# Kernel tuning notes

Hardware: AMD Instinct MI355X
Metric: run time of the kernel (lower is better)

## Reference

```python
import jax, jax.numpy as jnp
import numpy as np

B, N, D = 8, 2048, 256
K = 8
NP = 1024  # num_pooled = ceil(N * 0.5)
EPS = 1e-8
TEMP = 1.0


def setup_inputs() -> dict:
    key = jax.random.key(0)
    k1, k2, k3, k4 = jax.random.split(key, 4)
    tokens = jax.random.normal(k1, (B, N, D), dtype=jnp.float32)
    timestamps = jax.random.uniform(k2, (B, N), dtype=jnp.float32)
    W1 = jax.random.normal(k3, (2 * D, 128), dtype=jnp.float32) * 0.02
    b1 = jnp.zeros((128,), dtype=jnp.float32)
    W2 = jax.random.normal(k4, (128, NP), dtype=jnp.float32) * 0.02
    b2 = jnp.zeros((NP,), dtype=jnp.float32)
    return {"tokens": tokens, "timestamps": timestamps, "W1": W1, "b1": b1, "W2": W2, "b2": b2}


def _build_adjacency(tokens):
    # mutual-kNN graph on cosine similarity -> [B, N, N] float 0/1
    tn = tokens / (jnp.linalg.norm(tokens, axis=-1, keepdims=True) + EPS)
    sim = jnp.einsum("bnd,bmd->bnm", tn, tn)
    sim = jnp.where(jnp.eye(N, dtype=bool)[None], -jnp.inf, sim)  # no self (add_self=False)
    _, idx = jax.lax.top_k(sim, K)  # [B, N, K]
    bi = jnp.arange(B)[:, None, None]
    ri = jnp.arange(N)[None, :, None]
    adj = jnp.zeros((B, N, N), dtype=bool).at[bi, ri, idx].set(True)
    adj = adj & jnp.swapaxes(adj, 1, 2)  # mutual
    return adj.astype(jnp.float32)


def reference(tokens, timestamps, W1, b1, W2, b2):
    adjacency = _build_adjacency(tokens)

    # degree-normalized aggregation (use_gnn=True)
    degree = jnp.clip(adjacency.sum(axis=-1, keepdims=True), 1.0, None)
    agg = jnp.matmul(adjacency / degree, tokens)  # [B, N, D]
    features = jnp.concatenate([tokens, agg], axis=-1)  # [B, N, 2D]

    # assignment MLP (Linear -> exact GELU -> Linear), softmax over clusters
    h = jax.nn.gelu(features @ W1 + b1, approximate=False)
    logits = h @ W2 + b2  # [B, N, NP]
    assign = jax.nn.softmax(logits / TEMP, axis=-1)

    # soft-assignment pooling
    pooled_tokens = jnp.einsum("bnp,bnd->bpd", assign, tokens)  # [B, NP, D]
    pooled_t = jnp.einsum("bnp,bn->bp", assign, timestamps)  # [B, NP]

    # reorder pooled tokens by pooled timestamp
    sort_idx = jnp.argsort(pooled_t, axis=-1)
    pooled_tokens = jnp.take_along_axis(pooled_tokens, sort_idx[..., None], axis=1)
    pooled_t = jnp.take_along_axis(pooled_t, sort_idx, axis=1)

    # auxiliary losses
    assign_st = jnp.einsum("bnp,bmp->bnm", assign, assign)
    link_loss = jnp.mean((assign_st - adjacency) ** 2)
    entropy = jnp.mean(-jnp.sum(assign * jnp.log(assign + EPS), axis=-1))

    return pooled_tokens, pooled_t, link_loss, entropy
```

## Files before the change

### kernel.cpp

```cpp
#include <hip/hip_runtime.h>
#include <math.h>

#define B_ 8
#define N_ 2048
#define D_ 256
#define K_ 8
#define NP_ 1024
#define H_ 128
#define EPS_ 1e-8f
#define NEG_INF_ (-1e30f)

typedef unsigned int uint;
typedef unsigned short ushort;
typedef __attribute__((ext_vector_type(4))) float f32x4;
typedef __attribute__((ext_vector_type(8))) short short8;

__device__ __forceinline__ float gelu_exact(float x) {
    return 0.5f * x * (1.0f + erff(x * 0.70710678118654752440f));
}

__device__ __forceinline__ float dot4(float4 a, float4 b) {
    return a.x * b.x + a.y * b.y + a.z * b.z + a.w * b.w;
}

__device__ __forceinline__ ushort f2bf(float f) {
    uint u = __float_as_uint(f);
    u = (u + 0x7FFFu + ((u >> 16) & 1u)) >> 16;
    return (ushort)u;
}

__device__ __forceinline__ void gll16(const void* g, void* l) {
    __builtin_amdgcn_global_load_lds(
        (const __attribute__((address_space(1))) unsigned int*)g,
        (__attribute__((address_space(3))) unsigned int*)l, 16, 0, 0);
}

__device__ __forceinline__ float bsum256(float* red, int t, float v) {
    red[t] = v;
    __syncthreads();
#pragma unroll
    for (int s = 128; s > 0; s >>= 1) {
        if (t < s) red[t] += red[t + s];
        __syncthreads();
    }
    float r = red[0];
    __syncthreads();
    return r;
}

__device__ __forceinline__ float bmax256(float* red, int t, float v) {
    red[t] = v;
    __syncthreads();
#pragma unroll
    for (int s = 128; s > 0; s >>= 1) {
        if (t < s) red[t] = fmaxf(red[t], red[t + s]);
        __syncthreads();
    }
    float r = red[0];
    __syncthreads();
    return r;
}

__device__ __forceinline__ uint mono16(uint v) {
    return (v & 0x8000u) ? ((~v) & 0xFFFFu) : (v | 0x8000u);
}

__global__ __launch_bounds__(256) void k_norm(const float* __restrict__ tokens,
                                              float* __restrict__ tn,
                                              ushort* __restrict__ tnbf) {
    int row = blockIdx.x;
    int t = threadIdx.x;
    __shared__ float red[256];
    float x = tokens[(size_t)row * D_ + t];
    float ss = bsum256(red, t, x * x);
    float nrm = sqrtf(ss) + EPS_;
    float y = x / nrm;
    tn[(size_t)row * D_ + t] = y;
    tnbf[(size_t)row * D_ + t] = f2bf(y);
}

#define SCW_ 72
#define INSK_(L) { bool in_ = key > L; uint tm_ = L; L = in_ ? key : L; key = in_ ? tm_ : key; }
#define INS16_ INSK_(l0) INSK_(l1) INSK_(l2) INSK_(l3) INSK_(l4) INSK_(l5) INSK_(l6) INSK_(l7) \
               INSK_(l8) INSK_(l9) INSK_(l10) INSK_(l11) INSK_(l12) INSK_(l13) INSK_(l14) INSK_(l15)
#define INSM_ INSK_(m0) INSK_(m1) INSK_(m2) INSK_(m3) INSK_(m4) INSK_(m5) INSK_(m6) INSK_(m7) \
              INSK_(m8) INSK_(m9) INSK_(m10) INSK_(m11) INSK_(m12) INSK_(m13) INSK_(m14) INSK_(m15)

__global__ __launch_bounds__(256) void k_simtop(const ushort* __restrict__ tnbf,
                                                int* __restrict__ cands) {
    __shared__ __align__(16) char lds[43264];
    char* Bs = lds + 8192;
    ushort* sc = (ushort*)(lds + 40960);
    uint* mg = (uint*)(lds + 8192);

    int bid = blockIdx.x;
    int b = bid & 7;
    int panel = bid >> 3;
    int i0 = panel * 16;
    int t = threadIdx.x;
    int lane = t & 63;
    int wv = t >> 6;
    const char* tbb = (const char*)(tnbf + (size_t)b * N_ * D_);

#pragma unroll
    for (int c = 0; c < 2; ++c) {
        int e = (wv * 2 + c) * 64 + lane;
        int row = e >> 5, g = e & 31;
        gll16(tbb + (size_t)(i0 + row) * 512 + ((g ^ (row & 15)) << 4),
              lds + (wv * 2 + c) * 1024);
    }
#pragma unroll
    for (int c = 0; c < 8; ++c) {
        int e = (wv * 8 + c) * 64 + lane;
        int row = e >> 5, g = e & 31;
        gll16(tbb + (size_t)row * 512 + ((g ^ (row & 15)) << 4),
              Bs + (wv * 8 + c) * 1024);
    }
    asm volatile("s_waitcnt vmcnt(0)" ::: "memory");
    __syncthreads();

    int selrow = t >> 4;
    int selcs = t & 15;
    int gi = i0 + selrow;
    uint l0=0,l1=0,l2=0,l3=0,l4=0,l5=0,l6=0,l7=0,l8=0,l9=0,l10=0,l11=0,l12=0,l13=0,l14=0,l15=0;

    int arow = lane & 15;
    int brow = wv * 16 + (lane & 15);
    int scw = ((lane >> 4) * 4) * SCW_ + wv * 16 + (lane & 15);

    for (int jt = 0; jt < 32; ++jt) {
        f32x4 acc = (f32x4){0.f, 0.f, 0.f, 0.f};
#pragma unroll
        for (int ks = 0; ks < 8; ++ks) {
            int u = ks * 4 + (lane >> 4);
            short8 af = *(const short8*)(lds + arow * 512 + ((u ^ arow) << 4));
            short8 bf = *(const short8*)(Bs + brow * 512 + ((u ^ (lane & 15)) << 4));
            acc = __builtin_amdgcn_mfma_f32_16x16x32_bf16(af, bf, acc, 0, 0, 0);
        }
#pragma unroll
        for (int v = 0; v < 4; ++v) sc[scw + v * SCW_] = f2bf(acc[v]);
        __syncthreads();

        if (jt < 31) {
#pragma unroll
            for (int c = 0; c < 8; ++c) {
                int e = (wv * 8 + c) * 64 + lane;
                int row = e >> 5, g = e & 31;
                gll16(tbb + (size_t)((jt + 1) * 64 + row) * 512 + ((g ^ (row & 15)) << 4),
                      Bs + (wv * 8 + c) * 1024);
            }
        }
        int j0 = jt * 64;
        int sbase = selrow * SCW_;
#pragma unroll
        for (int jj = 0; jj < 4; ++jj) {
            int col = selcs + jj * 16;
            int j = j0 + col;
            uint sv = sc[sbase + col];
            if (j != gi) {
                uint key = (mono16(sv) << 16) | (65535u - (uint)j);
                if (key > l15) { INS16_ }
            }
        }
        asm volatile("s_waitcnt vmcnt(0)" ::: "memory");
        __syncthreads();
    }

    uint* ml = mg + (size_t)t * 17;
    ml[0]=l0; ml[1]=l1; ml[2]=l2; ml[3]=l3; ml[4]=l4; ml[5]=l5; ml[6]=l6; ml[7]=l7;
    ml[8]=l8; ml[9]=l9; ml[10]=l10; ml[11]=l11; ml[12]=l12; ml[13]=l13; ml[14]=l14; ml[15]=l15;
    __syncthreads();
    if (selcs == 0) {
        uint m0=0,m1=0,m2=0,m3=0,m4=0,m5=0,m6=0,m7=0,m8=0,m9=0,m10=0,m11=0,m12=0,m13=0,m14=0,m15=0;
        const uint* base = mg + (size_t)(selrow * 16) * 17;
#pragma unroll
        for (int s2 = 0; s2 < 16; ++s2) {
            const uint* lp = base + s2 * 17;
            for (int q = 0; q < 16; ++q) {
                uint key = lp[q];
                if (key <= m15) break;
                INSM_
            }
        }
        int* crow = cands + ((size_t)b * N_ + gi) * 16;
        crow[0]=(int)(65535u-(m0&0xFFFFu));   crow[1]=(int)(65535u-(m1&0xFFFFu));
        crow[2]=(int)(65535u-(m2&0xFFFFu));   crow[3]=(int)(65535u-(m3&0xFFFFu));
        crow[4]=(int)(65535u-(m4&0xFFFFu));   crow[5]=(int)(65535u-(m5&0xFFFFu));
        crow[6]=(int)(65535u-(m6&0xFFFFu));   crow[7]=(int)(65535u-(m7&0xFFFFu));
        crow[8]=(int)(65535u-(m8&0xFFFFu));   crow[9]=(int)(65535u-(m9&0xFFFFu));
        crow[10]=(int)(65535u-(m10&0xFFFFu)); crow[11]=(int)(65535u-(m11&0xFFFFu));
        crow[12]=(int)(65535u-(m12&0xFFFFu)); crow[13]=(int)(65535u-(m13&0xFFFFu));
        crow[14]=(int)(65535u-(m14&0xFFFFu)); crow[15]=(int)(65535u-(m15&0xFFFFu));
    }
}

__global__ __launch_bounds__(64) void k_rescore(const float* __restrict__ tn,
                                                const int* __restrict__ cands,
                                                int* __restrict__ topk) {
    int row = blockIdx.x;
    int b = row >> 11;
    int lane = threadIdx.x;
    int j = cands[(size_t)row * 16 + (lane & 15)];
    float s = 0.f;
    if (lane < 16) {
        const float* ti = tn + (size_t)row * D_;
        const float* tj = tn + ((size_t)(b << 11) + j) * D_;
        for (int d = 0; d < D_; d += 4) {
            float4 u = *(const float4*)(tj + d);
            float4 w = *(const float4*)(ti + d);
            s += dot4(u, w);
        }
    }
    float dv[16];
    int jv[16];
#pragma unroll
    for (int c = 0; c < 16; ++c) {
        dv[c] = __shfl(s, c);
        jv[c] = __shfl(j, c);
    }
    uint used = 0;
    for (int r = 0; r < 8; ++r) {
        float bv = -1e38f;
        int bj = 1 << 30, bc = -1;
#pragma unroll
        for (int c = 0; c < 16; ++c) {
            bool av = !(used & (1u << c));
            bool better = av && (dv[c] > bv || (dv[c] == bv && jv[c] < bj));
            bv = better ? dv[c] : bv;
            bj = better ? jv[c] : bj;
            bc = better ? c : bc;
        }
        used |= 1u << bc;
        if (lane == 0) topk[(size_t)row * K_ + r] = bj;
    }
}

__global__ __launch_bounds__(64) void k_adj_agg(const float* __restrict__ tokens,
                                                const int* __restrict__ topk,
                                                int* __restrict__ nbr,
                                                int* __restrict__ deg,
                                                float* __restrict__ agg) {
    int row = blockIdx.x;
    int b = row >> 11;
    int i = row & (N_ - 1);
    int t = threadIdx.x;
    __shared__ int s_cand[K_];
    __shared__ int s_nbr[K_];
    __shared__ int s_deg;
    if (t < K_) {
        int j = topk[(size_t)row * K_ + t];
        const int* tj = topk + ((size_t)(b * N_ + j)) * K_;
        bool mut = false;
#pragma unroll
        for (int k = 0; k < K_; ++k) mut = mut || (tj[k] == i);
        s_cand[t] = mut ? j : -1;
    }
    __syncthreads();
    if (t == 0) {
        int d = 0;
#pragma unroll
        for (int k = 0; k < K_; ++k)
            if (s_cand[k] >= 0) s_nbr[d++] = s_cand[k];
        s_deg = d;
    }
    __syncthreads();
    int dgi = s_deg;
    const float* tb = tokens + (size_t)b * N_ * D_;
    float a0 = 0, a1 = 0, a2 = 0, a3 = 0;
    for (int k = 0; k < dgi; ++k) {
        float4 v = *(const float4*)(tb + (size_t)s_nbr[k] * D_ + t * 4);
        a0 += v.x; a1 += v.y; a2 += v.z; a3 += v.w;
    }
    float inv = 1.0f / (float)(dgi > 0 ? dgi : 1);
    *(float4*)(agg + (size_t)row * D_ + t * 4) = make_float4(a0 * inv, a1 * inv, a2 * inv, a3 * inv);
    if (t < K_) nbr[(size_t)row * K_ + t] = (t < dgi) ? s_nbr[t] : -1;
    if (t == 0) deg[row] = dgi;
}

__global__ __launch_bounds__(256) void k_tokT(const float* __restrict__ tokens,
                                              ushort* __restrict__ tokT) {
    int b = blockIdx.z;
    int n0 = blockIdx.x * 32, d0 = blockIdx.y * 32;
    __shared__ float tile[32][33];
    int t = threadIdx.x;
#pragma unroll
    for (int q = 0; q < 4; ++q) {
        int e = q * 256 + t;
        int r = e >> 5, c = e & 31;
        tile[r][c] = tokens[((size_t)b * N_ + n0 + r) * D_ + d0 + c];
    }
    __syncthreads();
#pragma unroll
    for (int q = 0; q < 4; ++q) {
        int e = q * 256 + t;
        int r = e >> 5, c = e & 31;
        tokT[((size_t)b * D_ + d0 + r) * N_ + n0 + c] = f2bf(tile[c][r]);
    }
}

__global__ __launch_bounds__(256) void k_asT(const float* __restrict__ assign,
                                             ushort* __restrict__ assignT) {
    int b = blockIdx.z;
    int n0 = blockIdx.x * 32, p0 = blockIdx.y * 32;
    __shared__ float tile[32][33];
    int t = threadIdx.x;
#pragma unroll
    for (int q = 0; q < 4; ++q) {
        int e = q * 256 + t;
        int r = e >> 5, c = e & 31;
        tile[r][c] = assign[((size_t)b * N_ + n0 + r) * NP_ + p0 + c];
    }
    __syncthreads();
#pragma unroll
    for (int q = 0; q < 4; ++q) {
        int e = q * 256 + t;
        int r = e >> 5, c = e & 31;
        assignT[((size_t)b * NP_ + p0 + r) * N_ + n0 + c] = f2bf(tile[c][r]);
    }
}

__global__ __launch_bounds__(256) void k_mlp1(const float* __restrict__ tokens,
                                              const float* __restrict__ agg,
                                              const float* __restrict__ W1,
                                              const float* __restrict__ b1,
                                              float* __restrict__ h) {
    int row0 = blockIdx.x * 16;
    int t = threadIdx.x;
    int col = t & 127;
    int half = t >> 7;
    __shared__ float feat[16][2 * D_];
    for (int e = t; e < 16 * 2 * D_; e += 256) {
        int r = e >> 9, c = e & 511;
        feat[r][c] = (c < D_) ? tokens[(size_t)(row0 + r) * D_ + c]
                              : agg[(size_t)(row0 + r) * D_ + (c - D_)];
    }
    __syncthreads();
    const float* fr = &feat[half * 8][0];
    float bias = b1[col];
    float a0 = bias, a1 = bias, a2 = bias, a3 = bias, a4 = bias, a5 = bias, a6 = bias, a7 = bias;
    for (int i = 0; i < 2 * D_; i += 4) {
        float w0 = W1[(size_t)(i + 0) * H_ + col];
        float w1 = W1[(size_t)(i + 1) * H_ + col];
        float w2 = W1[(size_t)(i + 2) * H_ + col];
        float w3 = W1[(size_t)(i + 3) * H_ + col];
        float4 f0 = *(const float4*)(fr + 0 * 512 + i);
        float4 f1 = *(const float4*)(fr + 1 * 512 + i);
        float4 f2 = *(const float4*)(fr + 2 * 512 + i);
        float4 f3 = *(const float4*)(fr + 3 * 512 + i);
        float4 f4 = *(const float4*)(fr + 4 * 512 + i);
        float4 f5 = *(const float4*)(fr + 5 * 512 + i);
        float4 f6 = *(const float4*)(fr + 6 * 512 + i);
        float4 f7 = *(const float4*)(fr + 7 * 512 + i);
        a0 += f0.x * w0; a0 += f0.y * w1; a0 += f0.z * w2; a0 += f0.w * w3;
        a1 += f1.x * w0; a1 += f1.y * w1; a1 += f1.z * w2; a1 += f1.w * w3;
        a2 += f2.x * w0; a2 += f2.y * w1; a2 += f2.z * w2; a2 += f2.w * w3;
        a3 += f3.x * w0; a3 += f3.y * w1; a3 += f3.z * w2; a3 += f3.w * w3;
        a4 += f4.x * w0; a4 += f4.y * w1; a4 += f4.z * w2; a4 += f4.w * w3;
        a5 += f5.x * w0; a5 += f5.y * w1; a5 += f5.z * w2; a5 += f5.w * w3;
        a6 += f6.x * w0; a6 += f6.y * w1; a6 += f6.z * w2; a6 += f6.w * w3;
        a7 += f7.x * w0; a7 += f7.y * w1; a7 += f7.z * w2; a7 += f7.w * w3;
    }
    int rb = row0 + half * 8;
    h[(size_t)(rb + 0) * H_ + col] = gelu_exact(a0);
    h[(size_t)(rb + 1) * H_ + col] = gelu_exact(a1);
    h[(size_t)(rb + 2) * H_ + col] = gelu_exact(a2);
    h[(size_t)(rb + 3) * H_ + col] = gelu_exact(a3);
    h[(size_t)(rb + 4) * H_ + col] = gelu_exact(a4);
    h[(size_t)(rb + 5) * H_ + col] = gelu_exact(a5);
    h[(size_t)(rb + 6) * H_ + col] = gelu_exact(a6);
    h[(size_t)(rb + 7) * H_ + col] = gelu_exact(a7);
}

__global__ __launch_bounds__(256) void k_mlp2f(const float* __restrict__ hmat,
                                               const float* __restrict__ W2,
                                               const float* __restrict__ b2,
                                               float* __restrict__ assign,
                                               float* __restrict__ ent_partial) {
    int row0 = blockIdx.x * 16;
    int t = threadIdx.x;
    __shared__ float hsT[128 * 17];
    __shared__ float red2[16][256];
    __shared__ float red[256];
    for (int e = t; e < 16 * H_; e += 256) {
        int r = e >> 7, i = e & 127;
        hsT[i * 17 + r] = hmat[(size_t)row0 * H_ + e];
    }
    __syncthreads();
    float acc[16][4];
#pragma unroll
    for (int s = 0; s < 4; ++s) {
        float bb = b2[s * 256 + t];
#pragma unroll
        for (int r = 0; r < 16; ++r) acc[r][s] = bb;
    }
#pragma unroll 2
    for (int i = 0; i < H_; ++i) {
        float w0 = W2[(size_t)i * NP_ + t];
        float w1 = W2[(size_t)i * NP_ + 256 + t];
        float w2 = W2[(size_t)i * NP_ + 512 + t];
        float w3 = W2[(size_t)i * NP_ + 768 + t];
        float hv[16];
        *(float4*)&hv[0] = *(const float4*)&hsT[i * 17 + 0];
        *(float4*)&hv[4] = *(const float4*)&hsT[i * 17 + 4];
        *(float4*)&hv[8] = *(const float4*)&hsT[i * 17 + 8];
        *(float4*)&hv[12] = *(const float4*)&hsT[i * 17 + 12];
#pragma unroll
        for (int r = 0; r < 16; ++r) {
            acc[r][0] += hv[r] * w0; acc[r][1] += hv[r] * w1;
            acc[r][2] += hv[r] * w2; acc[r][3] += hv[r] * w3;
        }
    }
#pragma unroll
    for (int r = 0; r < 16; ++r)
        red2[r][t] = fmaxf(fmaxf(acc[r][0], acc[r][1]), fmaxf(acc[r][2], acc[r][3]));
    __syncthreads();
#pragma unroll
    for (int s = 128; s > 0; s >>= 1) {
        if (t < s) {
#pragma unroll
            for (int r = 0; r < 16; ++r) red2[r][t] = fmaxf(red2[r][t], red2[r][t + s]);
        }
        __syncthreads();
    }
#pragma unroll
    for (int r = 0; r < 16; ++r) {
        float m = red2[r][0];
        acc[r][0] -= m; acc[r][1] -= m; acc[r][2] -= m; acc[r][3] -= m;
    }
    __syncthreads();
#pragma unroll
    for (int r = 0; r < 16; ++r)
        red2[r][t] = expf(acc[r][0]) + expf(acc[r][1]) + expf(acc[r][2]) + expf(acc[r][3]);
    __syncthreads();
#pragma unroll
    for (int s = 128; s > 0; s >>= 1) {
        if (t < s) {
#pragma unroll
            for (int r = 0; r < 16; ++r) red2[r][t] += red2[r][t + s];
        }
        __syncthreads();
    }
    float entv = 0.f;
#pragma unroll
    for (int r = 0; r < 16; ++r) {
        float tot = red2[r][0];
        float inv = 1.0f / tot;
        float p0 = expf(acc[r][0]) * inv, p1 = expf(acc[r][1]) * inv;
        float p2 = expf(acc[r][2]) * inv, p3 = expf(acc[r][3]) * inv;
        float* arow = assign + (size_t)(row0 + r) * NP_;
        arow[t] = p0; arow[256 + t] = p1; arow[512 + t] = p2; arow[768 + t] = p3;
        entv -= p0 * logf(p0 + EPS_) + p1 * logf(p1 + EPS_) + p2 * logf(p2 + EPS_) + p3 * logf(p3 + EPS_);
    }
    float bs = bsum256(red, t, entv);
    if (t == 0) ent_partial[blockIdx.x] = bs;
}

__device__ __forceinline__ void stage8k(const ushort* __restrict__ A,
                                        const ushort* __restrict__ B,
                                        int kb, char* lA, char* lB, int wv, int lane) {
#pragma unroll
    for (int c = 0; c < 2; ++c) {
        int e = (wv * 2 + c) * 64 + lane;
        int row = e >> 3, g = e & 7;
        size_t go = (size_t)row * N_ + kb + ((g ^ (row & 7)) << 3);
        gll16(A + go, lA + (wv * 2 + c) * 1024);
        gll16(B + go, lB + (wv * 2 + c) * 1024);
    }
}

__device__ __forceinline__ void gemm64g(const ushort* __restrict__ A,
                                        const ushort* __restrict__ B,
                                        f32x4 acc[2][2], char* lds) {
    int t = threadIdx.x;
    int lane = t & 63;
    int wv = t >> 6;
    int wm = wv >> 1, wn = wv & 1;
    stage8k(A, B, 0, lds, lds + 8192, wv, lane);
    for (int kb = 0; kb < N_; kb += 64) {
        int cur = (kb >> 6) & 1;
        char* lA = lds + cur * 16384;
        char* lB = lA + 8192;
        asm volatile("s_waitcnt vmcnt(0)" ::: "memory");
        __syncthreads();
        if (kb + 64 < N_) {
            char* nA = lds + (cur ^ 1) * 16384;
            stage8k(A, B, kb + 64, nA, nA + 8192, wv, lane);
        }
#pragma unroll
        for (int ks = 0; ks < 2; ++ks) {
            short8 afr[2], bfr[2];
#pragma unroll
            for (int f = 0; f < 2; ++f) {
                int rowA = wm * 32 + f * 16 + (lane & 15);
                int u = ks * 4 + (lane >> 4);
                afr[f] = *(const short8*)(lA + rowA * 128 + ((u ^ (rowA & 7)) << 4));
                int rowB = wn * 32 + f * 16 + (lane & 15);
                bfr[f] = *(const short8*)(lB + rowB * 128 + ((u ^ (rowB & 7)) << 4));
            }
#pragma unroll
            for (int fm = 0; fm < 2; ++fm)
#pragma unroll
                for (int fn = 0; fn < 2; ++fn)
                    acc[fm][fn] = __builtin_amdgcn_mfma_f32_16x16x32_bf16(
                        afr[fm], bfr[fn], acc[fm][fn], 0, 0, 0);
        }
    }
}

__global__ __launch_bounds__(256) void k_pool64(const ushort* __restrict__ assignT,
                                                const ushort* __restrict__ tokT,
                                                float* __restrict__ pooled) {
    __shared__ __align__(16) char lds[32768];
    int bid = blockIdx.x;
    int b = bid & 7;
    int tile = bid >> 3;
    int p0 = (tile >> 2) * 64, d0 = (tile & 3) * 64;
    const ushort* A = assignT + ((size_t)b * NP_ + p0) * N_;
    const ushort* Bp = tokT + ((size_t)b * D_ + d0) * N_;
    f32x4 acc[2][2];
#pragma unroll
    for (int x = 0; x < 2; ++x)
#pragma unroll
        for (int y = 0; y < 2; ++y) acc[x][y] = (f32x4){0.f, 0.f, 0.f, 0.f};
    gemm64g(A, Bp, acc, lds);
    int lane = threadIdx.x & 63;
    int wid = threadIdx.x >> 6;
    int wm = wid >> 1, wn = wid & 1;
#pragma unroll
    for (int fm = 0; fm < 2; ++fm)
#pragma unroll
        for (int fn = 0; fn < 2; ++fn) {
            int p = p0 + wm * 32 + fm * 16 + (lane >> 4) * 4;
            int d = d0 + wn * 32 + fn * 16 + (lane & 15);
#pragma unroll
            for (int v = 0; v < 4; ++v)
                pooled[((size_t)b * NP_ + p + v) * D_ + d] = acc[fm][fn][v];
        }
}

__global__ __launch_bounds__(256) void k_gram64(const ushort* __restrict__ assignT,
                                                float* __restrict__ gram_partial) {
    __shared__ __align__(16) char lds[32768];
    __shared__ float red[256];
    int bid = blockIdx.x;
    int b = bid & 7;
    int idx = bid >> 3;
    int ti = 0, rem = idx;
    while (rem >= 16 - ti) { rem -= 16 - ti; ++ti; }
    int tj = ti + rem;
    const ushort* A = assignT + ((size_t)b * NP_ + ti * 64) * N_;
    const ushort* Bp = assignT + ((size_t)b * NP_ + tj * 64) * N_;
    f32x4 acc[2][2];
#pragma unroll
    for (int x = 0; x < 2; ++x)
#pragma unroll
        for (int y = 0; y < 2; ++y) acc[x][y] = (f32x4){0.f, 0.f, 0.f, 0.f};
    gemm64g(A, Bp, acc, lds);
    float lsum = 0.f;
#pragma unroll
    for (int x = 0; x < 2; ++x)
#pragma unroll
        for (int y = 0; y < 2; ++y)
#pragma unroll
            for (int v = 0; v < 4; ++v) lsum += acc[x][y][v] * acc[x][y][v];
    float bs = bsum256(red, threadIdx.x, lsum);
    if (threadIdx.x == 0) gram_partial[(size_t)b * 136 + idx] = (ti == tj ? 1.0f : 2.0f) * bs;
}

__global__ __launch_bounds__(256) void k_poolt_part(const float* __restrict__ assign,
                                                    const float* __restrict__ ts,
                                                    float* __restrict__ part) {
    int bid = blockIdx.x;
    int b = bid & 7, ck = bid >> 3;
    int t = threadIdx.x;
    const float* A = assign + ((size_t)b * N_ + (size_t)ck * 64) * NP_;
    const float* T = ts + (size_t)b * N_ + (size_t)ck * 64;
    float4 acc = make_float4(0.f, 0.f, 0.f, 0.f);
    for (int n = 0; n < 64; ++n) {
        float4 v = *(const float4*)(A + (size_t)n * NP_ + t * 4);
        float tv = T[n];
        acc.x += v.x * tv; acc.y += v.y * tv; acc.z += v.z * tv; acc.w += v.w * tv;
    }
    *(float4*)(part + ((size_t)(b * 32 + ck)) * NP_ + t * 4) = acc;
}

__global__ __launch_bounds__(256) void k_poolt_red(const float* __restrict__ part,
                                                   float* __restrict__ pooled_t_u) {
    int b = blockIdx.x;
    int t = threadIdx.x;
    float4 acc = make_float4(0.f, 0.f, 0.f, 0.f);
    for (int ck = 0; ck < 32; ++ck) {
        float4 v = *(const float4*)(part + ((size_t)(b * 32 + ck)) * NP_ + t * 4);
        acc.x += v.x; acc.y += v.y; acc.z += v.z; acc.w += v.w;
    }
    *(float4*)(pooled_t_u + (size_t)b * NP_ + t * 4) = acc;
}

__global__ __launch_bounds__(64) void k_edge(const float* __restrict__ assign,
                                             const int* __restrict__ nbr,
                                             const int* __restrict__ deg,
                                             float* __restrict__ edge_partial) {
    int row = blockIdx.x;
    int t = threadIdx.x;
    int dgi = deg[row];
    int b = row >> 11;
    float acc = 0.f;
    if (dgi > 0) {
        const float* ai = assign + (size_t)row * NP_;
        float areg[16];
#pragma unroll
        for (int q = 0; q < 16; ++q) areg[q] = ai[q * 64 + t];
        for (int k = 0; k < dgi; ++k) {
            int j = nbr[(size_t)row * K_ + k];
            const float* aj = assign + ((size_t)(b * N_ + j)) * NP_;
#pragma unroll
            for (int q = 0; q < 16; ++q) acc += areg[q] * aj[q * 64 + t];
        }
    }
#pragma unroll
    for (int s = 32; s > 0; s >>= 1) acc += __shfl_down(acc, s);
    if (t == 0) edge_partial[row] = acc;
}

__global__ __launch_bounds__(256) void k_sort(const float* __restrict__ pooled_t_u,
                                              float* __restrict__ out_pt,
                                              int* __restrict__ sortidx) {
    int b = blockIdx.x;
    int t = threadIdx.x;
    __shared__ float val[NP_];
    __shared__ int sidx[NP_];
    for (int e = t; e < NP_; e += 256) { val[e] = pooled_t_u[(size_t)b * NP_ + e]; sidx[e] = e; }
    __syncthreads();
    for (int k = 2; k <= NP_; k <<= 1) {
        for (int j = k >> 1; j > 0; j >>= 1) {
            for (int e = t; e < NP_; e += 256) {
                int l = e ^ j;
                if (l > e) {
                    bool up = ((e & k) == 0);
                    float v1 = val[e], v2 = val[l];
                    int i1 = sidx[e], i2 = sidx[l];
                    bool sw = up ? ((v1 > v2) || (v1 == v2 && i1 > i2))
                                 : ((v1 < v2) || (v1 == v2 && i1 < i2));
                    if (sw) { val[e] = v2; val[l] = v1; sidx[e] = i2; sidx[l] = i1; }
                }
            }
            __syncthreads();
        }
    }
    for (int e = t; e < NP_; e += 256) {
        out_pt[(size_t)b * NP_ + e] = val[e];
        sortidx[(size_t)b * NP_ + e] = sidx[e];
    }
}

__global__ __launch_bounds__(64) void k_gather(const float* __restrict__ pooledU,
                                               const int* __restrict__ sortidx,
                                               float* __restrict__ out) {
    int bp = blockIdx.x;
    int b = bp >> 10;
    int src = sortidx[bp];
    const float4* s = (const float4*)(pooledU + ((size_t)(b << 10) + src) * D_);
    float4* d = (float4*)(out + (size_t)bp * D_);
    d[threadIdx.x] = s[threadIdx.x];
}

__global__ __launch_bounds__(256) void k_fin(const float* __restrict__ gram_partial,
                                             const float* __restrict__ edge_partial,
                                             const float* __restrict__ ent_partial,
                                             const int* __restrict__ deg,
                                             float* __restrict__ out2) {
    int t = threadIdx.x;
    __shared__ float red[256];
    float t1 = 0.f, t2 = 0.f, t3 = 0.f, ent = 0.f;
    for (int i = t; i < 136 * B_; i += 256) t1 += gram_partial[i];
    for (int i = t; i < B_ * N_; i += 256) t2 += edge_partial[i];
    for (int i = t; i < (B_ * N_) / 16; i += 256) ent += ent_partial[i];
    for (int i = t; i < B_ * N_; i += 256) t3 += (float)deg[i];
    t1 = bsum256(red, t, t1);
    t2 = bsum256(red, t, t2);
    t3 = bsum256(red, t, t3);
    ent = bsum256(red, t, ent);
    if (t == 0) {
        out2[0] = (t1 - 2.f * t2 + t3) / (float)((size_t)B_ * N_ * N_);
        out2[1] = ent / (float)(B_ * N_);
    }
}

extern "C" void kernel_launch(void* const* d_in, const int* in_sizes, int n_in,
                              void* d_out, int out_size, void* d_ws, size_t ws_size,
                              hipStream_t stream) {
    const float* tokens = (const float*)d_in[0];
    const float* tstamp = (const float*)d_in[1];
    const float* W1 = (const float*)d_in[2];
    const float* b1 = (const float*)d_in[3];
    const float* W2 = (const float*)d_in[4];
    const float* b2 = (const float*)d_in[5];
    float* out = (float*)d_out;

    char* wsp = (char*)d_ws;
    size_t off = 0;
    auto alloc = [&](size_t bytes) -> void* {
        void* p = wsp + off;
        off += (bytes + 255) & ~(size_t)255;
        return p;
    };
    float* tn = (float*)alloc(sizeof(float) * (size_t)B_ * N_ * D_);
    float* agg = tn;
    float* assign = (float*)alloc(sizeof(float) * (size_t)B_ * N_ * NP_);
    ushort* tnbf = (ushort*)alloc(sizeof(ushort) * (size_t)B_ * N_ * D_);
    ushort* tokT = tnbf;
    float* hbuf = (float*)alloc(sizeof(float) * (size_t)B_ * N_ * H_);
    ushort* assignT = (ushort*)alloc(sizeof(ushort) * (size_t)B_ * NP_ * N_);
    float* pooledU = (float*)alloc(sizeof(float) * (size_t)B_ * NP_ * D_);
    float* pooltU = (float*)alloc(sizeof(float) * (size_t)B_ * NP_);
    float* poolt_part = (float*)alloc(sizeof(float) * (size_t)B_ * 32 * NP_);
    int* candbuf = (int*)alloc(sizeof(int) * (size_t)B_ * N_ * 16);
    int* topkbuf = (int*)alloc(sizeof(int) * (size_t)B_ * N_ * K_);
    int* nbrbuf = (int*)alloc(sizeof(int) * (size_t)B_ * N_ * K_);
    int* degbuf = (int*)alloc(sizeof(int) * (size_t)B_ * N_);
    int* sortidx = (int*)alloc(sizeof(int) * (size_t)B_ * NP_);
    float* gram_p = (float*)alloc(sizeof(float) * 136 * B_);
    float* edge_p = (float*)alloc(sizeof(float) * (size_t)B_ * N_);
    float* ent_p = (float*)alloc(sizeof(float) * (size_t)(B_ * N_) / 16);

    k_norm<<<B_ * N_, 256, 0, stream>>>(tokens, tn, tnbf);
    k_simtop<<<1024, 256, 0, stream>>>(tnbf, candbuf);
    k_rescore<<<B_ * N_, 64, 0, stream>>>(tn, candbuf, topkbuf);
    k_adj_agg<<<B_ * N_, 64, 0, stream>>>(tokens, topkbuf, nbrbuf, degbuf, agg);
    k_tokT<<<dim3(N_ / 32, D_ / 32, B_), 256, 0, stream>>>(tokens, tokT);
    k_mlp1<<<(B_ * N_) / 16, 256, 0, stream>>>(tokens, agg, W1, b1, hbuf);
    k_mlp2f<<<(B_ * N_) / 16, 256, 0, stream>>>(hbuf, W2, b2, assign, ent_p);
    k_asT<<<dim3(N_ / 32, NP_ / 32, B_), 256, 0, stream>>>(assign, assignT);
    k_pool64<<<512, 256, 0, stream>>>(assignT, tokT, pooledU);
    k_poolt_part<<<256, 256, 0, stream>>>(assign, tstamp, poolt_part);
    k_poolt_red<<<B_, 256, 0, stream>>>(poolt_part, pooltU);
    k_gram64<<<1088, 256, 0, stream>>>(assignT, gram_p);
    k_edge<<<B_ * N_, 64, 0, stream>>>(assign, nbrbuf, degbuf, edge_p);
    k_sort<<<B_, 256, 0, stream>>>(pooltU, out + (size_t)B_ * NP_ * D_, sortidx);
    k_gather<<<B_ * NP_, 64, 0, stream>>>(pooledU, sortidx, out);
    k_fin<<<1, 256, 0, stream>>>(gram_p, edge_p, ent_p, degbuf,
                                 out + (size_t)B_ * NP_ * D_ + (size_t)B_ * NP_);
}
```

Before: 604.5 us.

## Process 32 query rows per simtop block with shared top-k threshold gating

k_simtop now handles 32 query rows per block instead of 16. Each wave computes a 16x32 tile with two MFMAs per A fragment, so every loaded column panel is reused across twice as many rows and the grid is halved. Each row's 8 selector threads share a running 16th-best threshold via shuffles to skip insertions early, and global source pointers are precomputed and advanced instead of recomputed each tile. Separately, k_mlp2f pads its transposed LDS tile stride from 17 to 20 so the float4 reads are aligned, and raises the unroll factor; the extra LDS and registers may reduce occupancy.

```diff
diff --git a/kernel.cpp b/kernel.cpp
--- a/kernel.cpp
+++ b/kernel.cpp
@@ -88,79 +88,101 @@
 
 __global__ __launch_bounds__(256) void k_simtop(const ushort* __restrict__ tnbf,
                                                 int* __restrict__ cands) {
-    __shared__ __align__(16) char lds[43264];
-    char* Bs = lds + 8192;
-    ushort* sc = (ushort*)(lds + 40960);
-    uint* mg = (uint*)(lds + 8192);
+    __shared__ __align__(16) char lds[53760];
+    char* Bs = lds + 16384;
+    ushort* sc = (ushort*)(lds + 49152);
+    uint* mg = (uint*)(lds + 16384);
 
     int bid = blockIdx.x;
     int b = bid & 7;
     int panel = bid >> 3;
-    int i0 = panel * 16;
+    int i0 = panel * 32;
     int t = threadIdx.x;
     int lane = t & 63;
     int wv = t >> 6;
+    int rh = wv & 1, ch = wv >> 1;
     const char* tbb = (const char*)(tnbf + (size_t)b * N_ * D_);
 
 #pragma unroll
-    for (int c = 0; c < 2; ++c) {
-        int e = (wv * 2 + c) * 64 + lane;
+    for (int c = 0; c < 4; ++c) {
+        int e = (wv * 4 + c) * 64 + lane;
         int row = e >> 5, g = e & 31;
         gll16(tbb + (size_t)(i0 + row) * 512 + ((g ^ (row & 15)) << 4),
-              lds + (wv * 2 + c) * 1024);
-    }
+              lds + (wv * 4 + c) * 1024);
+    }
+    const char* gsrc[8];
 #pragma unroll
     for (int c = 0; c < 8; ++c) {
         int e = (wv * 8 + c) * 64 + lane;
         int row = e >> 5, g = e & 31;
-        gll16(tbb + (size_t)row * 512 + ((g ^ (row & 15)) << 4),
-              Bs + (wv * 8 + c) * 1024);
+        gsrc[c] = tbb + (size_t)row * 512 + ((g ^ (row & 15)) << 4);
+    }
+#pragma unroll
+    for (int c = 0; c < 8; ++c) {
+        gll16(gsrc[c], Bs + (wv * 8 + c) * 1024);
+        gsrc[c] += 32768;
     }
     asm volatile("s_waitcnt vmcnt(0)" ::: "memory");
     __syncthreads();
 
-    int selrow = t >> 4;
-    int selcs = t & 15;
+    int selrow = t >> 3;
+    int selcs = t & 7;
     int gi = i0 + selrow;
     uint l0=0,l1=0,l2=0,l3=0,l4=0,l5=0,l6=0,l7=0,l8=0,l9=0,l10=0,l11=0,l12=0,l13=0,l14=0,l15=0;
-
-    int arow = lane & 15;
-    int brow = wv * 16 + (lane & 15);
-    int scw = ((lane >> 4) * 4) * SCW_ + wv * 16 + (lane & 15);
+    uint rth = 0;
+
+    int arow = rh * 16 + (lane & 15);
+    int brow0 = ch * 32 + (lane & 15);
+    int brow1 = brow0 + 16;
+    int scw = (rh * 16 + (lane >> 4) * 4) * SCW_ + ch * 32 + (lane & 15);
 
     for (int jt = 0; jt < 32; ++jt) {
-        f32x4 acc = (f32x4){0.f, 0.f, 0.f, 0.f};
+        f32x4 acc0 = (f32x4){0.f, 0.f, 0.f, 0.f};
+        f32x4 acc1 = (f32x4){0.f, 0.f, 0.f, 0.f};
 #pragma unroll
         for (int ks = 0; ks < 8; ++ks) {
             int u = ks * 4 + (lane >> 4);
-            short8 af = *(const short8*)(lds + arow * 512 + ((u ^ arow) << 4));
-            short8 bf = *(const short8*)(Bs + brow * 512 + ((u ^ (lane & 15)) << 4));
-            acc = __builtin_amdgcn_mfma_f32_16x16x32_bf16(af, bf, acc, 0, 0, 0);
-        }
-#pragma unroll
-        for (int v = 0; v < 4; ++v) sc[scw + v * SCW_] = f2bf(acc[v]);
+            short8 af = *(const short8*)(lds + arow * 512 + ((u ^ (arow & 15)) << 4));
+            short8 bf0 = *(const short8*)(Bs + brow0 * 512 + ((u ^ (lane & 15)) << 4));
+            short8 bf1 = *(const short8*)(Bs + brow1 * 512 + ((u ^ (lane & 15)) << 4));
+            acc0 = __builtin_amdgcn_mfma_f32_16x16x32_bf16(af, bf0, acc0, 0, 0, 0);
+            acc1 = __builtin_amdgcn_mfma_f32_16x16x32_bf16(af, bf1, acc1, 0, 0, 0);
+        }
+#pragma unroll
+        for (int v = 0; v < 4; ++v) sc[scw + v * SCW_] = f2bf(acc0[v]);
+#pragma unroll
+        for (int v = 0; v < 4; ++v) sc[scw + v * SCW_ + 16] = f2bf(acc1[v]);
         __syncthreads();
 
         if (jt < 31) {
 #pragma unroll
             for (int c = 0; c < 8; ++c) {
-                int e = (wv * 8 + c) * 64 + lane;
-                int row = e >> 5, g = e & 31;
-                gll16(tbb + (size_t)((jt + 1) * 64 + row) * 512 + ((g ^ (row & 15)) << 4),
-                      Bs + (wv * 8 + c) * 1024);
+                gll16(gsrc[c], Bs + (wv * 8 + c) * 1024);
+                gsrc[c] += 32768;
             }
         }
         int j0 = jt * 64;
         int sbase = selrow * SCW_;
-#pragma unroll
-        for (int jj = 0; jj < 4; ++jj) {
-            int col = selcs + jj * 16;
+        uint gate = l15 > rth ? l15 : rth;
+#pragma unroll
+        for (int jj = 0; jj < 8; ++jj) {
+            int col = selcs + jj * 8;
             int j = j0 + col;
             uint sv = sc[sbase + col];
             if (j != gi) {
                 uint key = (mono16(sv) << 16) | (65535u - (uint)j);
-                if (key > l15) { INS16_ }
+                if (key > gate) {
+                    INS16_
+                    gate = l15 > rth ? l15 : rth;
+                }
             }
+        }
+        {
+            uint m = l15;
+            m = m > (uint)__shfl_xor((int)m, 1) ? m : (uint)__shfl_xor((int)m, 1);
+            m = m > (uint)__shfl_xor((int)m, 2) ? m : (uint)__shfl_xor((int)m, 2);
+            m = m > (uint)__shfl_xor((int)m, 4) ? m : (uint)__shfl_xor((int)m, 4);
+            rth = m;
         }
         asm volatile("s_waitcnt vmcnt(0)" ::: "memory");
         __syncthreads();
@@ -172,9 +194,9 @@
     __syncthreads();
     if (selcs == 0) {
         uint m0=0,m1=0,m2=0,m3=0,m4=0,m5=0,m6=0,m7=0,m8=0,m9=0,m10=0,m11=0,m12=0,m13=0,m14=0,m15=0;
-        const uint* base = mg + (size_t)(selrow * 16) * 17;
-#pragma unroll
-        for (int s2 = 0; s2 < 16; ++s2) {
+        const uint* base = mg + (size_t)(selrow * 8) * 17;
+#pragma unroll
+        for (int s2 = 0; s2 < 8; ++s2) {
             const uint* lp = base + s2 * 17;
             for (int q = 0; q < 16; ++q) {
                 uint key = lp[q];
@@ -378,12 +400,12 @@
                                                float* __restrict__ ent_partial) {
     int row0 = blockIdx.x * 16;
     int t = threadIdx.x;
-    __shared__ float hsT[128 * 17];
+    __shared__ float hsT[128 * 20];
     __shared__ float red2[16][256];
     __shared__ float red[256];
     for (int e = t; e < 16 * H_; e += 256) {
         int r = e >> 7, i = e & 127;
-        hsT[i * 17 + r] = hmat[(size_t)row0 * H_ + e];
+        hsT[i * 20 + r] = hmat[(size_t)row0 * H_ + e];
     }
     __syncthreads();
     float acc[16][4];
@@ -393,17 +415,17 @@
 #pragma unroll
         for (int r = 0; r < 16; ++r) acc[r][s] = bb;
     }
-#pragma unroll 2
+#pragma unroll 4
     for (int i = 0; i < H_; ++i) {
         float w0 = W2[(size_t)i * NP_ + t];
         float w1 = W2[(size_t)i * NP_ + 256 + t];
         float w2 = W2[(size_t)i * NP_ + 512 + t];
         float w3 = W2[(size_t)i * NP_ + 768 + t];
         float hv[16];
-        *(float4*)&hv[0] = *(const float4*)&hsT[i * 17 + 0];
-        *(float4*)&hv[4] = *(const float4*)&hsT[i * 17 + 4];
-        *(float4*)&hv[8] = *(const float4*)&hsT[i * 17 + 8];
-        *(float4*)&hv[12] = *(const float4*)&hsT[i * 17 + 12];
+        *(float4*)&hv[0] = *(const float4*)&hsT[i * 20 + 0];
+        *(float4*)&hv[4] = *(const float4*)&hsT[i * 20 + 4];
+        *(float4*)&hv[8] = *(const float4*)&hsT[i * 20 + 8];
+        *(float4*)&hv[12] = *(const float4*)&hsT[i * 20 + 12];
 #pragma unroll
         for (int r = 0; r < 16; ++r) {
             acc[r][0] += hv[r] * w0; acc[r][1] += hv[r] * w1;
@@ -724,7 +746,7 @@
     float* ent_p = (float*)alloc(sizeof(float) * (size_t)(B_ * N_) / 16);
 
     k_norm<<<B_ * N_, 256, 0, stream>>>(tokens, tn, tnbf);
-    k_simtop<<<1024, 256, 0, stream>>>(tnbf, candbuf);
+    k_simtop<<<512, 256, 0, stream>>>(tnbf, candbuf);
     k_rescore<<<B_ * N_, 64, 0, stream>>>(tn, candbuf, topkbuf);
     k_adj_agg<<<B_ * N_, 64, 0, stream>>>(tokens, topkbuf, nbrbuf, degbuf, agg);
     k_tokT<<<dim3(N_ / 32, D_ / 32, B_), 256, 0, stream>>>(tokens, tokT);
```

After: 588.1 us (median of 2 runs). 1.03x faster.
